# Optimization experiments

Measured on AMD Instinct MI355X. Metric: run time of the kernel, lower is better.

Reference implementation:

```python
import jax, jax.numpy as jnp
import numpy as np
from jax import lax

B, T, I, H = 64, 512, 256, 512


def _lstm_cell(inp, h, c, Wx, bx, Wh):
    # Wx: (4, in_dim, H), bx: (4, H), Wh: (4, H, H); gate order: i, f, o, g
    gates = jnp.einsum('bi,gio->bgo', inp, Wx) + jnp.einsum('bh,gho->bgo', h, Wh) + bx
    i_t = jax.nn.sigmoid(gates[:, 0])
    f_t = jax.nn.sigmoid(gates[:, 1])
    o_t = jax.nn.sigmoid(gates[:, 2])
    g_t = jnp.tanh(gates[:, 3])
    c_new = f_t * c + i_t * g_t
    h_new = o_t * jnp.tanh(c_new)
    return h_new, c_new


def setup_inputs() -> dict:
    key = jax.random.key(0)
    ks = jax.random.split(key, 9)
    s_i = 1.0 / np.sqrt(H)  # nn.Linear default init scale (uniform fan_in)
    s_x0 = 1.0 / np.sqrt(I)
    u = lambda k, shape, s: jax.random.uniform(k, shape, jnp.float32, -s, s)
    return {
        'x':   jax.random.normal(ks[0], (B, T, I), jnp.float32),
        'Wx0': u(ks[1], (4, I, H), s_x0),
        'bx0': u(ks[2], (4, H), s_x0),
        'Wh0': u(ks[3], (4, H, H), s_i),
        'Wx1': u(ks[4], (4, H, H), s_i),
        'bx1': u(ks[5], (4, H), s_i),
        'Wh1': u(ks[6], (4, H, H), s_i),
        'Wfc': u(ks[7], (H, 1), s_i),
        'bfc': u(ks[8], (1,), s_i),
    }


def reference(x, Wx0, bx0, Wh0, Wx1, bx1, Wh1, Wfc, bfc):
    b = x.shape[0]
    h = Wh0.shape[-1]
    zeros = jnp.zeros((b, h), x.dtype)
    carry0 = (zeros, zeros, zeros, zeros)  # h0, c0, h1, c1

    def step(carry, x_t):
        h0, c0, h1, c1 = carry
        h0, c0 = _lstm_cell(x_t, h0, c0, Wx0, bx0, Wh0)
        h1, c1 = _lstm_cell(h0, h1, c1, Wx1, bx1, Wh1)
        return (h0, c0, h1, c1), None

    x_t_major = jnp.swapaxes(x, 0, 1)  # (T, B, I)
    (h0, c0, h1, c1), _ = lax.scan(step, carry0, x_t_major)
    return h1 @ Wfc + bfc  # (B, 1)
```

## Files before the change

kernel.cpp:

```cpp
#include <hip/hip_runtime.h>
#include <stdint.h>

#define B_ 64
#define T_ 512
#define I_ 256
#define H_ 512
#define NTHR_ 512
#define D_ 8

typedef __attribute__((ext_vector_type(8))) short short8;
typedef __attribute__((ext_vector_type(4))) float float4v;
typedef __attribute__((ext_vector_type(4))) unsigned int uint4v;

static_assert(sizeof(short8) == 16, "");

#define TILE_B 2048
#define SLOT_B ((size_t)4 * 16 * TILE_B)

__device__ __forceinline__ unsigned short f2bf(float x) {
  union { float f; uint32_t u; } v; v.f = x;
  uint32_t r = v.u + 0x7FFFu + ((v.u >> 16) & 1u);
  return (unsigned short)(r >> 16);
}
__device__ __forceinline__ float bf2f(unsigned short h) {
  union { uint32_t u; float f; } v; v.u = ((uint32_t)h) << 16; return v.f;
}
__device__ __forceinline__ void splitHL(float x, unsigned short& hi, unsigned short& lo) {
  hi = f2bf(x);
  lo = f2bf(x - bf2f(hi));
}

__device__ __forceinline__ size_t rbyte(int slot, int bg, int ht) {
  return ((size_t)slot * 64 + bg * 16 + ht) * TILE_B;
}

__device__ __forceinline__ void wait_ge(const uint32_t* p, int tgt) {
  if (tgt <= 0) return;
  int it = 0;
  while ((int)__hip_atomic_load(p, __ATOMIC_RELAXED, __HIP_MEMORY_SCOPE_AGENT) < tgt) {
    __builtin_amdgcn_s_sleep(1);
    if (++it > 2000000) break;
  }
}

__device__ __forceinline__ short8 mk8(uint32_t a0, uint32_t a1, uint32_t b0, uint32_t b1) {
  union { uint32_t u[4]; short8 s; } t;
  t.u[0] = a0; t.u[1] = a1; t.u[2] = b0; t.u[3] = b1;
  return t.s;
}

#define MFMA16(A, Bv, C) __builtin_amdgcn_mfma_f32_16x16x32_bf16(A, Bv, C, 0, 0, 0)

#define WAITV(n) do { \
    asm volatile("s_waitcnt vmcnt(" #n ")" ::: "memory"); \
    __builtin_amdgcn_sched_barrier(0); \
  } while (0)

template <int LAYER, bool FULL>
__device__ void run_layer(
    int a,
    const float* __restrict__ x,
    const float* __restrict__ Wxp, const float* __restrict__ bxp,
    const float* __restrict__ Whp,
    uint32_t* prog0, uint32_t* prog1,
    uint8_t* r0, uint8_t* r1,
    float* h1f,
    unsigned short* Wsh, float* red)
{
  constexpr int K1 = LAYER ? H_ : I_;
  constexpr int NT = (K1 + H_) / 32;
  constexpr int NTT = NT / 2;
  const int tid = threadIdx.x;
  const int lane = tid & 63;
  const int wid = tid >> 6;
  const int bg = wid & 3;
  const int kh = wid >> 2;
  const int qq = lane >> 4;
  const int cc = lane & 15;
  const int brow = bg * 16 + cc;

  short8 wlo[NTT];
  for (int pass = 0; pass < 2; ++pass) {
    for (int idx = tid; idx < NT * 512; idx += NTHR_) {
      int tile = idx >> 9, r = idx & 511, ln = r >> 3, j = r & 7;
      int k = tile * 32 + 4 * (ln >> 4) + (j & 3) + 16 * (j >> 2);
      int n = 4 * a + (ln & 3);
      int g = (ln & 15) >> 2;
      float wvv = (k < K1) ? Wxp[((size_t)g * K1 + k) * H_ + n]
                           : Whp[((size_t)g * H_ + (k - K1)) * H_ + n];
      unsigned short hi, lo; splitHL(wvv, hi, lo);
      Wsh[idx] = pass ? hi : lo;
    }
    __syncthreads();
    if (pass == 0) {
      #pragma unroll
      for (int tt = 0; tt < NTT; ++tt) {
        int tile = 2 * tt + kh;
        wlo[tt] = *(const short8*)(Wsh + tile * 512 + lane * 8);
      }
      __syncthreads();
    }
  }

  const float biasv = bxp[(size_t)(cc >> 2) * H_ + 4 * a + (cc & 3)];
  float cst[4] = {0.f, 0.f, 0.f, 0.f};

  uint32_t* myprog = LAYER ? prog1 : prog0;
  const bool ownw = FULL ? ((tid & 127) == a) : false;

  for (int t = 0; t < T_; ++t) {
    const int slotP = FULL ? t       : (t & (D_ - 1));
    const int slotC = FULL ? (t + 1) : ((t + 1) & (D_ - 1));
    const float bv = (kh == 0) ? biasv : 0.f;
    float4v accA = {bv, bv, bv, bv};
    float4v accB = {0.f, 0.f, 0.f, 0.f};
    float4v accC = {0.f, 0.f, 0.f, 0.f};

    uint4v X0[8], X1[8];

    auto issue_ring = [&](int tt) {
      const int tile = 2 * tt + kh;
      const uint8_t* p;
      if (!LAYER)         p = r0 + rbyte(slotP, bg, tile - 8);
      else if (tile < 16) p = r0 + rbyte(slotC, bg, tile);
      else                p = r1 + rbyte(slotP, bg, tile - 16);
      p += (size_t)lane * 16;
      const int s = tt & 7;
      if constexpr (FULL) {
        asm volatile("global_load_dwordx4 %0, %2, off\n\t"
                     "global_load_dwordx4 %1, %2, off offset:1024"
                     : "=&v"(X0[s]), "=&v"(X1[s]) : "v"(p) : "memory");
      } else {
        asm volatile("global_load_dwordx4 %0, %2, off sc0 sc1\n\t"
                     "global_load_dwordx4 %1, %2, off offset:1024 sc0 sc1"
                     : "=&v"(X0[s]), "=&v"(X1[s]) : "v"(p) : "memory");
      }
    };
    auto proc_ring = [&](int tt) {
      const int tile = 2 * tt + kh;
      const int s = tt & 7;
      short8 h = mk8(X0[s][0], X0[s][1], X1[s][0], X1[s][1]);
      short8 l = mk8(X0[s][2], X0[s][3], X1[s][2], X1[s][3]);
      short8 bhi = *(const short8*)(Wsh + tile * 512 + lane * 8);
      accA = MFMA16(h, bhi, accA);
      accB = MFMA16(l, bhi, accB);
      accC = MFMA16(h, wlo[tt], accC);
    };

    if constexpr (!LAYER) {
      uint4v xw0[4], xw1[4];
      #pragma unroll
      for (int u = 0; u < 4; ++u) {
        const float* xp = x + ((size_t)brow * T_ + t) * I_ + (2 * u + kh) * 32 + 4 * qq;
        asm volatile("global_load_dwordx4 %0, %2, off\n\t"
                     "global_load_dwordx4 %1, %2, off offset:64"
                     : "=&v"(xw0[u]), "=&v"(xw1[u]) : "v"(xp) : "memory");
      }
      if constexpr (FULL) {
        if (!ownw) wait_ge(&prog0[tid], t);
      } else {
        if (tid < 128)      wait_ge(&prog0[tid], t);
        else if (tid < 256) wait_ge(&prog1[tid - 128], t - (D_ - 1));
      }
      __syncthreads();
      #pragma unroll
      for (int tt = 4; tt < 12; ++tt) issue_ring(tt);
      WAITV(16);
      #pragma unroll
      for (int u = 0; u < 4; ++u) {
        short8 ahi, alo;
        #pragma unroll
        for (int j = 0; j < 4; ++j) {
          unsigned short hh, ll;
          splitHL(__uint_as_float(xw0[u][j]), hh, ll); ahi[j] = (short)hh; alo[j] = (short)ll;
          splitHL(__uint_as_float(xw1[u][j]), hh, ll); ahi[j + 4] = (short)hh; alo[j + 4] = (short)ll;
        }
        const int tile = 2 * u + kh;
        short8 bhi = *(const short8*)(Wsh + tile * 512 + lane * 8);
        accA = MFMA16(ahi, bhi, accA);
        accB = MFMA16(alo, bhi, accB);
        accC = MFMA16(ahi, wlo[u], accC);
      }
      WAITV(8);
      proc_ring(4); proc_ring(5); proc_ring(6); proc_ring(7);
      WAITV(0);
      proc_ring(8); proc_ring(9); proc_ring(10); proc_ring(11);
    } else {
      if constexpr (FULL) {
        wait_ge(&prog0[tid], t + 1);
        __syncthreads();
        #pragma unroll
        for (int tt = 0; tt < 8; ++tt) issue_ring(tt);
        WAITV(8);
        proc_ring(0); proc_ring(1); proc_ring(2); proc_ring(3);
        WAITV(0);
        proc_ring(4); proc_ring(5); proc_ring(6); proc_ring(7);
        if (!ownw) wait_ge(&prog1[tid], t);
        __syncthreads();
        #pragma unroll
        for (int tt = 8; tt < 16; ++tt) issue_ring(tt);
        WAITV(8);
        proc_ring(8); proc_ring(9); proc_ring(10); proc_ring(11);
        WAITV(0);
        proc_ring(12); proc_ring(13); proc_ring(14); proc_ring(15);
      } else {
        if (tid < 128)      wait_ge(&prog0[tid], t + 1);
        else if (tid < 256) wait_ge(&prog1[tid - 128], t);
        __syncthreads();
        #pragma unroll
        for (int tt = 0; tt < 8; ++tt) issue_ring(tt);
        WAITV(8);
        proc_ring(0); proc_ring(1); proc_ring(2); proc_ring(3);
        issue_ring(8); issue_ring(9); issue_ring(10); issue_ring(11);
        WAITV(8);
        proc_ring(4); proc_ring(5); proc_ring(6); proc_ring(7);
        issue_ring(12); issue_ring(13); issue_ring(14); issue_ring(15);
        WAITV(8);
        proc_ring(8); proc_ring(9); proc_ring(10); proc_ring(11);
        WAITV(0);
        proc_ring(12); proc_ring(13); proc_ring(14); proc_ring(15);
      }
    }

    float4v acc = accA + accB + accC;

    if (kh == 1) *(float4v*)(red + ((bg << 6) + lane) * 4) = acc;
    __syncthreads();
    if (kh == 0) {
      acc += *(const float4v*)(red + ((bg << 6) + lane) * 4);

      const bool isg = cc >= 12;
      float av[4];
      #pragma unroll
      for (int i = 0; i < 4; ++i) {
        float xg = acc[i];
        float arg = isg ? xg + xg : xg;
        float e = __expf(-fabsf(arg));
        float s = (arg >= 0.f) ? 1.f / (1.f + e) : e / (1.f + e);
        av[i] = isg ? (s + s - 1.f) : s;
      }
      float hn[4];
      #pragma unroll
      for (int i = 0; i < 4; ++i) {
        float fv = __shfl_xor(av[i], 4);
        float ov = __shfl_xor(av[i], 8);
        float gv = __shfl_xor(av[i], 12);
        float cn = fv * cst[i] + av[i] * gv;
        cst[i] = cn;
        float e2 = __expf(-2.f * fabsf(cn));
        float th = (1.f - e2) / (1.f + e2);
        hn[i] = ov * ((cn >= 0.f) ? th : -th);
      }
      float v0[4], v1[4], v2[4], v3[4];
      #pragma unroll
      for (int d = 0; d < 4; ++d) {
        int src = (lane & 0x30) | d;
        v0[d] = __shfl(hn[0], src);
        v1[d] = __shfl(hn[1], src);
        v2[d] = __shfl(hn[2], src);
        v3[d] = __shfl(hn[3], src);
      }
      if (cc < 4) {
        unsigned short hh[4], ll[4]; float4v hf;
        #pragma unroll
        for (int d = 0; d < 4; ++d) {
          float hv = (cc == 0) ? v0[d] : (cc == 1) ? v1[d] : (cc == 2) ? v2[d] : v3[d];
          hf[d] = hv;
          splitHL(hv, hh[d], ll[d]);
        }
        uint4v pk;
        pk[0] = (uint32_t)hh[0] | ((uint32_t)hh[1] << 16);
        pk[1] = (uint32_t)hh[2] | ((uint32_t)hh[3] << 16);
        pk[2] = (uint32_t)ll[0] | ((uint32_t)ll[1] << 16);
        pk[3] = (uint32_t)ll[2] | ((uint32_t)ll[3] << 16);
        uint8_t* dstb = (LAYER ? r1 : r0) + rbyte(slotC, bg, a >> 3)
                      + (size_t)((a >> 2) & 1) * 1024
                      + (size_t)(16 * (a & 3) + 4 * qq + cc) * 16;
        asm volatile("global_store_dwordx4 %0, %1, off sc0 sc1"
                     :: "v"(dstb), "v"(pk) : "memory");
        if (LAYER && t == T_ - 1) {
          float4v* hp = (float4v*)(h1f + (size_t)(bg * 16 + 4 * qq + cc) * H_ + 4 * a);
          asm volatile("global_store_dwordx4 %0, %1, off sc0 sc1"
                       :: "v"(hp), "v"(hf) : "memory");
        }
      }
    }
    if constexpr (FULL) {
      if (kh == 0) {
        asm volatile("s_waitcnt vmcnt(0)" ::: "memory");
        if (lane == 0)
          __hip_atomic_store(&myprog[bg * 128 + a], (uint32_t)(t + 1),
                             __ATOMIC_RELAXED, __HIP_MEMORY_SCOPE_AGENT);
      }
      __syncthreads();
    } else {
      asm volatile("s_waitcnt vmcnt(0)" ::: "memory");
      __syncthreads();
      if (tid == 0)
        __hip_atomic_store(&myprog[a], (uint32_t)(t + 1),
                           __ATOMIC_RELAXED, __HIP_MEMORY_SCOPE_AGENT);
    }
  }
}

template <bool FULL>
__global__ __launch_bounds__(NTHR_, 2) void lstm_persist(
    const float* __restrict__ x,
    const float* __restrict__ Wx0, const float* __restrict__ bx0, const float* __restrict__ Wh0,
    const float* __restrict__ Wx1, const float* __restrict__ bx1, const float* __restrict__ Wh1,
    uint32_t* prog0, uint32_t* prog1,
    uint8_t* ring0, uint8_t* ring1,
    float* h1f)
{
  __shared__ unsigned short Wsh[16384];
  __shared__ float red[1024];
  if (blockIdx.x < 128)
    run_layer<0, FULL>(blockIdx.x, x, Wx0, bx0, Wh0, prog0, prog1, ring0, ring1, h1f, Wsh, red);
  else
    run_layer<1, FULL>(blockIdx.x - 128, x, Wx1, bx1, Wh1, prog0, prog1, ring0, ring1, h1f, Wsh, red);
}

__global__ void fc_out(const float* __restrict__ h1f, const float* __restrict__ Wfc,
                       const float* __restrict__ bfc, float* __restrict__ out)
{
  int tid = threadIdx.x;
  int b = tid >> 3, p = tid & 7;
  const float* hp = h1f + (size_t)b * H_ + p * 64;
  const float* wp = Wfc + p * 64;
  float4v hv[16];
  #pragma unroll
  for (int q = 0; q < 16; ++q)
    asm volatile("global_load_dwordx4 %0, %1, off sc0 sc1"
                 : "=&v"(hv[q]) : "v"(hp + 4 * q) : "memory");
  asm volatile("s_waitcnt vmcnt(0)" ::: "memory");
  float s = 0.f;
  #pragma unroll
  for (int q = 0; q < 16; ++q) {
    float4v wv = *(const float4v*)(wp + 4 * q);
    s += hv[q][0] * wv[0] + hv[q][1] * wv[1] + hv[q][2] * wv[2] + hv[q][3] * wv[3];
  }
  s += __shfl_xor(s, 1);
  s += __shfl_xor(s, 2);
  s += __shfl_xor(s, 4);
  if (p == 0) out[b] = s + bfc[0];
}

extern "C" void kernel_launch(void* const* d_in, const int* in_sizes, int n_in,
                              void* d_out, int out_size, void* d_ws, size_t ws_size,
                              hipStream_t stream)
{
  const float* x   = (const float*)d_in[0];
  const float* Wx0 = (const float*)d_in[1];
  const float* bx0 = (const float*)d_in[2];
  const float* Wh0 = (const float*)d_in[3];
  const float* Wx1 = (const float*)d_in[4];
  const float* bx1 = (const float*)d_in[5];
  const float* Wh1 = (const float*)d_in[6];
  const float* Wfc = (const float*)d_in[7];
  const float* bfc = (const float*)d_in[8];

  uint8_t* ws = (uint8_t*)d_ws;
  const size_t RINGB_FULL = (size_t)(T_ + 1) * SLOT_B;
  const size_t RINGB_CYC  = (size_t)D_ * SLOT_B;
  const size_t NEED_FULL  = 4096 + 2 * RINGB_FULL + (size_t)B_ * H_ * 4;

  uint32_t* prog0 = (uint32_t*)ws;
  uint32_t* prog1 = (uint32_t*)(ws + 2048);

  if (ws_size >= NEED_FULL) {
    uint8_t* ring0 = ws + 4096;
    uint8_t* ring1 = ws + 4096 + RINGB_FULL;
    float* h1f = (float*)(ws + 4096 + 2 * RINGB_FULL);
    (void)hipMemsetAsync(ws, 0, 4096 + SLOT_B, stream);
    (void)hipMemsetAsync(ring1, 0, SLOT_B, stream);
    hipLaunchKernelGGL(lstm_persist<true>, dim3(256), dim3(NTHR_), 0, stream,
                       x, Wx0, bx0, Wh0, Wx1, bx1, Wh1,
                       prog0, prog1, ring0, ring1, h1f);
    hipLaunchKernelGGL(fc_out, dim3(1), dim3(512), 0, stream,
                       h1f, Wfc, bfc, (float*)d_out);
  } else {
    uint8_t* ring0 = ws + 4096;
    uint8_t* ring1 = ws + 4096 + RINGB_CYC;
    float* h1f = (float*)(ws + 4096 + 2 * RINGB_CYC);
    (void)hipMemsetAsync(ws, 0, 4096 + 2 * RINGB_CYC, stream);
    hipLaunchKernelGGL(lstm_persist<false>, dim3(256), dim3(NTHR_), 0, stream,
                       x, Wx0, bx0, Wh0, Wx1, bx1, Wh1,
                       prog0, prog1, ring0, ring1, h1f);
    hipLaunchKernelGGL(fc_out, dim3(1), dim3(512), 0, stream,
                       h1f, Wfc, bfc, (float*)d_out);
  }
}
```

Baseline: 3.118 ms.

## Prepack x into bf16 hi/lo ring tiles and restructure layer loads

A new prep kernel converts x into the same bf16 hi/lo tiled layout used by the recurrent ring, so layer 0 loads pre-split tiles with the ring path instead of splitting fp32 values inside the serial recurrence. Layer 1 in full mode now issues both ring halves before the second dependency wait and interleaves loads with MFMA processing. The spin-wait polls without sleeping for the first iterations to cut wake-up latency. It costs an extra pass over x and more workspace, and only runs when the workspace is large enough.

```diff
diff --git a/kernel.cpp b/kernel.cpp
--- a/kernel.cpp
+++ b/kernel.cpp
@@ -38,8 +38,8 @@
   if (tgt <= 0) return;
   int it = 0;
   while ((int)__hip_atomic_load(p, __ATOMIC_RELAXED, __HIP_MEMORY_SCOPE_AGENT) < tgt) {
-    __builtin_amdgcn_s_sleep(1);
     if (++it > 2000000) break;
+    if (it > 32) __builtin_amdgcn_s_sleep(1);
   }
 }
 
@@ -56,10 +56,11 @@
     __builtin_amdgcn_sched_barrier(0); \
   } while (0)
 
-template <int LAYER, bool FULL>
+template <int LAYER, bool FULL, bool XPK>
 __device__ void run_layer(
     int a,
     const float* __restrict__ x,
+    const uint8_t* __restrict__ xpk,
     const float* __restrict__ Wxp, const float* __restrict__ bxp,
     const float* __restrict__ Whp,
     uint32_t* prog0, uint32_t* prog1,
@@ -136,6 +137,15 @@
                      : "=&v"(X0[s]), "=&v"(X1[s]) : "v"(p) : "memory");
       }
     };
+    auto issue_x = [&](int tt) {
+      const int tile = 2 * tt + kh;
+      const uint8_t* p = xpk + (((size_t)t * 4 + bg) * 8 + tile) * TILE_B
+                       + (size_t)lane * 16;
+      const int s = tt & 7;
+      asm volatile("global_load_dwordx4 %0, %2, off\n\t"
+                   "global_load_dwordx4 %1, %2, off offset:1024"
+                   : "=&v"(X0[s]), "=&v"(X1[s]) : "v"(p) : "memory");
+    };
     auto proc_ring = [&](int tt) {
       const int tile = 2 * tt + kh;
       const int s = tt & 7;
@@ -148,57 +158,75 @@
     };
 
     if constexpr (!LAYER) {
-      uint4v xw0[4], xw1[4];
-      #pragma unroll
-      for (int u = 0; u < 4; ++u) {
-        const float* xp = x + ((size_t)brow * T_ + t) * I_ + (2 * u + kh) * 32 + 4 * qq;
-        asm volatile("global_load_dwordx4 %0, %2, off\n\t"
-                     "global_load_dwordx4 %1, %2, off offset:64"
-                     : "=&v"(xw0[u]), "=&v"(xw1[u]) : "v"(xp) : "memory");
-      }
-      if constexpr (FULL) {
-        if (!ownw) wait_ge(&prog0[tid], t);
+      if constexpr (XPK) {
+        #pragma unroll
+        for (int tt = 0; tt < 4; ++tt) issue_x(tt);
+        if constexpr (FULL) {
+          if (!ownw) wait_ge(&prog0[tid], t);
+        }
+        __syncthreads();
+        #pragma unroll
+        for (int tt = 4; tt < 8; ++tt) issue_ring(tt);
+        WAITV(8);
+        proc_ring(0); proc_ring(1); proc_ring(2); proc_ring(3);
+        issue_ring(8); issue_ring(9); issue_ring(10); issue_ring(11);
+        WAITV(8);
+        proc_ring(4); proc_ring(5); proc_ring(6); proc_ring(7);
+        WAITV(0);
+        proc_ring(8); proc_ring(9); proc_ring(10); proc_ring(11);
       } else {
-        if (tid < 128)      wait_ge(&prog0[tid], t);
-        else if (tid < 256) wait_ge(&prog1[tid - 128], t - (D_ - 1));
-      }
-      __syncthreads();
-      #pragma unroll
-      for (int tt = 4; tt < 12; ++tt) issue_ring(tt);
-      WAITV(16);
-      #pragma unroll
-      for (int u = 0; u < 4; ++u) {
-        short8 ahi, alo;
-        #pragma unroll
-        for (int j = 0; j < 4; ++j) {
-          unsigned short hh, ll;
-          splitHL(__uint_as_float(xw0[u][j]), hh, ll); ahi[j] = (short)hh; alo[j] = (short)ll;
-          splitHL(__uint_as_float(xw1[u][j]), hh, ll); ahi[j + 4] = (short)hh; alo[j + 4] = (short)ll;
-        }
-        const int tile = 2 * u + kh;
-        short8 bhi = *(const short8*)(Wsh + tile * 512 + lane * 8);
-        accA = MFMA16(ahi, bhi, accA);
-        accB = MFMA16(alo, bhi, accB);
-        accC = MFMA16(ahi, wlo[u], accC);
-      }
-      WAITV(8);
-      proc_ring(4); proc_ring(5); proc_ring(6); proc_ring(7);
-      WAITV(0);
-      proc_ring(8); proc_ring(9); proc_ring(10); proc_ring(11);
+        uint4v xw0[4], xw1[4];
+        #pragma unroll
+        for (int u = 0; u < 4; ++u) {
+          const float* xp = x + ((size_t)brow * T_ + t) * I_ + (2 * u + kh) * 32 + 4 * qq;
+          asm volatile("global_load_dwordx4 %0, %2, off\n\t"
+                       "global_load_dwordx4 %1, %2, off offset:64"
+                       : "=&v"(xw0[u]), "=&v"(xw1[u]) : "v"(xp) : "memory");
+        }
+        if constexpr (FULL) {
+          if (!ownw) wait_ge(&prog0[tid], t);
+        } else {
+          if (tid < 128)      wait_ge(&prog0[tid], t);
+          else if (tid < 256) wait_ge(&prog1[tid - 128], t - (D_ - 1));
+        }
+        __syncthreads();
+        #pragma unroll
+        for (int tt = 4; tt < 12; ++tt) issue_ring(tt);
+        WAITV(16);
+        #pragma unroll
+        for (int u = 0; u < 4; ++u) {
+          short8 ahi, alo;
+          #pragma unroll
+          for (int j = 0; j < 4; ++j) {
+            unsigned short hh, ll;
+            splitHL(__uint_as_float(xw0[u][j]), hh, ll); ahi[j] = (short)hh; alo[j] = (short)ll;
+            splitHL(__uint_as_float(xw1[u][j]), hh, ll); ahi[j + 4] = (short)hh; alo[j + 4] = (short)ll;
+          }
+          const int tile = 2 * u + kh;
+          short8 bhi = *(const short8*)(Wsh + tile * 512 + lane * 8);
+          accA = MFMA16(ahi, bhi, accA);
+          accB = MFMA16(alo, bhi, accB);
+          accC = MFMA16(ahi, wlo[u], accC);
+        }
+        WAITV(8);
+        proc_ring(4); proc_ring(5); proc_ring(6); proc_ring(7);
+        WAITV(0);
+        proc_ring(8); proc_ring(9); proc_ring(10); proc_ring(11);
+      }
     } else {
       if constexpr (FULL) {
         wait_ge(&prog0[tid], t + 1);
         __syncthreads();
         #pragma unroll
         for (int tt = 0; tt < 8; ++tt) issue_ring(tt);
-        WAITV(8);
-        proc_ring(0); proc_ring(1); proc_ring(2); proc_ring(3);
-        WAITV(0);
-        proc_ring(4); proc_ring(5); proc_ring(6); proc_ring(7);
         if (!ownw) wait_ge(&prog1[tid], t);
         __syncthreads();
-        #pragma unroll
-        for (int tt = 8; tt < 16; ++tt) issue_ring(tt);
+        WAITV(8);
+        proc_ring(0); proc_ring(1); proc_ring(2); proc_ring(3);
+        issue_ring(8); issue_ring(9); issue_ring(10); issue_ring(11);
+        WAITV(8);
+        proc_ring(4); proc_ring(5); proc_ring(6); proc_ring(7);
+        issue_ring(12); issue_ring(13); issue_ring(14); issue_ring(15);
         WAITV(8);
         proc_ring(8); proc_ring(9); proc_ring(10); proc_ring(11);
         WAITV(0);
@@ -303,9 +331,9 @@
   }
 }
 
-template <bool FULL>
+template <bool FULL, bool XPK>
 __global__ __launch_bounds__(NTHR_, 2) void lstm_persist(
-    const float* __restrict__ x,
+    const float* __restrict__ x, const uint8_t* __restrict__ xpk,
     const float* __restrict__ Wx0, const float* __restrict__ bx0, const float* __restrict__ Wh0,
     const float* __restrict__ Wx1, const float* __restrict__ bx1, const float* __restrict__ Wh1,
     uint32_t* prog0, uint32_t* prog1,
@@ -315,9 +343,34 @@
   __shared__ unsigned short Wsh[16384];
   __shared__ float red[1024];
   if (blockIdx.x < 128)
-    run_layer<0, FULL>(blockIdx.x, x, Wx0, bx0, Wh0, prog0, prog1, ring0, ring1, h1f, Wsh, red);
+    run_layer<0, FULL, XPK>(blockIdx.x, x, xpk, Wx0, bx0, Wh0, prog0, prog1,
+                            ring0, ring1, h1f, Wsh, red);
   else
-    run_layer<1, FULL>(blockIdx.x - 128, x, Wx1, bx1, Wh1, prog0, prog1, ring0, ring1, h1f, Wsh, red);
+    run_layer<1, FULL, XPK>(blockIdx.x - 128, x, xpk, Wx1, bx1, Wh1, prog0, prog1,
+                            ring0, ring1, h1f, Wsh, red);
+}
+
+__global__ void prep_x(const float* __restrict__ x, uint8_t* __restrict__ xpk)
+{
+  size_t idx = (size_t)blockIdx.x * blockDim.x + threadIdx.x;
+  if (idx >= (size_t)T_ * 4 * 8 * 2 * 64) return;
+  int l    = idx & 63;
+  int jh   = (idx >> 6) & 1;
+  int tile = (idx >> 7) & 7;
+  int bg   = (idx >> 10) & 3;
+  int t    = (int)(idx >> 12);
+  int row  = bg * 16 + (l & 15);
+  int k0   = tile * 32 + 4 * (l >> 4) + 16 * jh;
+  float4v f = *(const float4v*)(x + ((size_t)row * T_ + t) * I_ + k0);
+  unsigned short hh[4], ll[4];
+  #pragma unroll
+  for (int d = 0; d < 4; ++d) splitHL(f[d], hh[d], ll[d]);
+  uint4v pk;
+  pk[0] = (uint32_t)hh[0] | ((uint32_t)hh[1] << 16);
+  pk[1] = (uint32_t)hh[2] | ((uint32_t)hh[3] << 16);
+  pk[2] = (uint32_t)ll[0] | ((uint32_t)ll[1] << 16);
+  pk[3] = (uint32_t)ll[2] | ((uint32_t)ll[3] << 16);
+  *(uint4v*)(xpk + idx * 16) = pk;
 }
 
 __global__ void fc_out(const float* __restrict__ h1f, const float* __restrict__ Wfc,
@@ -362,19 +415,35 @@
   uint8_t* ws = (uint8_t*)d_ws;
   const size_t RINGB_FULL = (size_t)(T_ + 1) * SLOT_B;
   const size_t RINGB_CYC  = (size_t)D_ * SLOT_B;
-  const size_t NEED_FULL  = 4096 + 2 * RINGB_FULL + (size_t)B_ * H_ * 4;
+  const size_t XPKB       = (size_t)T_ * 4 * 8 * TILE_B;
+  const size_t H1FB       = (size_t)B_ * H_ * 4;
+  const size_t NEED_FULL  = 4096 + 2 * RINGB_FULL + H1FB;
+  const size_t NEED_XPK   = NEED_FULL + XPKB;
 
   uint32_t* prog0 = (uint32_t*)ws;
   uint32_t* prog1 = (uint32_t*)(ws + 2048);
 
-  if (ws_size >= NEED_FULL) {
+  if (ws_size >= NEED_XPK) {
+    uint8_t* ring0 = ws + 4096;
+    uint8_t* ring1 = ws + 4096 + RINGB_FULL;
+    uint8_t* xpk   = ws + 4096 + 2 * RINGB_FULL;
+    float* h1f = (float*)(ws + 4096 + 2 * RINGB_FULL + XPKB);
+    (void)hipMemsetAsync(ws, 0, 4096 + SLOT_B, stream);
+    (void)hipMemsetAsync(ring1, 0, SLOT_B, stream);
+    hipLaunchKernelGGL(prep_x, dim3(4096), dim3(512), 0, stream, x, xpk);
+    hipLaunchKernelGGL((lstm_persist<true, true>), dim3(256), dim3(NTHR_), 0, stream,
+                       x, xpk, Wx0, bx0, Wh0, Wx1, bx1, Wh1,
+                       prog0, prog1, ring0, ring1, h1f);
+    hipLaunchKernelGGL(fc_out, dim3(1), dim3(512), 0, stream,
+                       h1f, Wfc, bfc, (float*)d_out);
+  } else if (ws_size >= NEED_FULL) {
     uint8_t* ring0 = ws + 4096;
     uint8_t* ring1 = ws + 4096 + RINGB_FULL;
     float* h1f = (float*)(ws + 4096 + 2 * RINGB_FULL);
     (void)hipMemsetAsync(ws, 0, 4096 + SLOT_B, stream);
     (void)hipMemsetAsync(ring1, 0, SLOT_B, stream);
-    hipLaunchKernelGGL(lstm_persist<true>, dim3(256), dim3(NTHR_), 0, stream,
-                       x, Wx0, bx0, Wh0, Wx1, bx1, Wh1,
+    hipLaunchKernelGGL((lstm_persist<true, false>), dim3(256), dim3(NTHR_), 0, stream,
+                       x, (const uint8_t*)nullptr, Wx0, bx0, Wh0, Wx1, bx1, Wh1,
                        prog0, prog1, ring0, ring1, h1f);
     hipLaunchKernelGGL(fc_out, dim3(1), dim3(512), 0, stream,
                        h1f, Wfc, bfc, (float*)d_out);
@@ -383,8 +452,8 @@
     uint8_t* ring1 = ws + 4096 + RINGB_CYC;
     float* h1f = (float*)(ws + 4096 + 2 * RINGB_CYC);
     (void)hipMemsetAsync(ws, 0, 4096 + 2 * RINGB_CYC, stream);
-    hipLaunchKernelGGL(lstm_persist<false>, dim3(256), dim3(NTHR_), 0, stream,
-                       x, Wx0, bx0, Wh0, Wx1, bx1, Wh1,
+    hipLaunchKernelGGL((lstm_persist<false, false>), dim3(256), dim3(NTHR_), 0, stream,
+                       x, (const uint8_t*)nullptr, Wx0, bx0, Wh0, Wx1, bx1, Wh1,
                        prog0, prog1, ring0, ring1, h1f);
     hipLaunchKernelGGL(fc_out, dim3(1), dim3(512), 0, stream,
                        h1f, Wfc, bfc, (float*)d_out);
```

After: 2.749 ms. 1.13x faster.
